# Kernel tuning notes

Measured on AMD Instinct MI355X. Metric: run time of the kernel, lower is better.

The kernel has to match this reference:

```python
import jax, jax.numpy as jnp
import numpy as np

NUM_ATTRS = 8    # A: number of attribute names in attr_map
NUM_VALS = 16    # V: number of distinct values per attribute


def setup_inputs() -> dict:
    key = jax.random.key(0)
    k1, k2 = jax.random.split(key)
    B, D = 2_000_000, 8
    predictions = jax.random.normal(k1, (B, D), dtype=jnp.float32)
    attr_vals = jax.random.randint(k2, (B, NUM_ATTRS), 0, NUM_VALS, dtype=jnp.int32)
    return {"predictions": predictions, "attr_vals": attr_vals}


def reference(predictions, attr_vals):
    B, A = attr_vals.shape
    V = NUM_VALS
    # per-node mean of sigmoid probs; stacking rows then .mean() == mean of per-node means
    per_node = jnp.mean(jax.nn.sigmoid(predictions), axis=1)  # [B]
    # flatten (attr, value) groups into A*V segments
    seg_ids = (attr_vals + jnp.arange(A, dtype=attr_vals.dtype)[None, :] * V).reshape(-1)  # [B*A]
    vals = jnp.broadcast_to(per_node[:, None], (B, A)).reshape(-1)  # [B*A]
    sums = jax.ops.segment_sum(vals, seg_ids, num_segments=A * V)
    counts = jax.ops.segment_sum(jnp.ones_like(vals), seg_ids, num_segments=A * V)
    means = (sums / jnp.maximum(counts, 1.0)).reshape(A, V)      # [A, V]
    present = (counts > 0).reshape(A, V)                          # [A, V]
    # pairwise squared diffs of group means within each attribute (i < j)
    diff = means[:, :, None] - means[:, None, :]                  # [A, V, V]
    triu = jnp.triu(jnp.ones((V, V), dtype=bool), k=1)
    pair_mask = present[:, :, None] & present[:, None, :] & triu[None, :, :]
    total_loss = jnp.sum(jnp.where(pair_mask, diff * diff, 0.0))
    num_comparisons = jnp.sum(pair_mask)
    return jnp.where(num_comparisons > 0, total_loss / num_comparisons, 0.0)
```

## Files before the change

### kernel.cpp

```cpp
#include <hip/hip_runtime.h>

#define NA 8
#define NV 16
#define NS (NA * NV)
#define NP 4
#define NJ 256
#define NE (NP * NJ)
#define FIX_SHIFT 43
#define FIX_MASK ((1ULL << FIX_SHIFT) - 1)
#define FIX_SCALE 2147483648.0f

__global__ __launch_bounds__(256) void k1_accum(
    const float4* __restrict__ preds4,
    const int4*   __restrict__ attrs4,
    unsigned long long* __restrict__ partials,
    int total4, int nb)
{
    __shared__ unsigned long long h[NE];
    for (int i = threadIdx.x; i < NE; i += 256) h[i] = 0ULL;
    __syncthreads();

    const int pbase = (threadIdx.x & 1) ? 2 * NJ : 0;
    const int stride = nb * 256;
    for (int idx = blockIdx.x * 256 + threadIdx.x; idx < total4; idx += stride) {
        float4 p = preds4[idx];
        int4   a = attrs4[idx];

        float half = __builtin_amdgcn_rcpf(1.0f + __expf(-p.x))
                   + __builtin_amdgcn_rcpf(1.0f + __expf(-p.y))
                   + __builtin_amdgcn_rcpf(1.0f + __expf(-p.z))
                   + __builtin_amdgcn_rcpf(1.0f + __expf(-p.w));
        float per_node = (half + __shfl_xor(half, 1)) * 0.125f;
        unsigned int fixed = (unsigned int)(per_node * FIX_SCALE);
        unsigned long long add = (1ULL << FIX_SHIFT) | (unsigned long long)fixed;

        atomicAdd(&h[pbase + ((a.x << 4) | a.y)], add);
        atomicAdd(&h[pbase + NJ + ((a.z << 4) | a.w)], add);
    }
    __syncthreads();

    unsigned long long* dst = partials + (size_t)blockIdx.x * NE;
    for (int i = threadIdx.x; i < NE; i += 256) {
        dst[i] = h[i];
    }
}

__global__ __launch_bounds__(256) void k2_reduce(
    const unsigned long long* __restrict__ partials,
    unsigned long long* __restrict__ jsum,
    unsigned int*       __restrict__ jcnt,
    int g)
{
    const unsigned long long* src = partials + (size_t)blockIdx.x * g * NE;
    unsigned long long s0 = 0, s1 = 0, s2 = 0, s3 = 0;
    unsigned int c0 = 0, c1 = 0, c2 = 0, c3 = 0;
    for (int b = 0; b < g; ++b) {
        const unsigned long long* s = src + (size_t)b * NE;
        unsigned long long p0 = s[threadIdx.x];
        unsigned long long p1 = s[threadIdx.x + 256];
        unsigned long long p2 = s[threadIdx.x + 512];
        unsigned long long p3 = s[threadIdx.x + 768];
        s0 += p0 & FIX_MASK; c0 += (unsigned int)(p0 >> FIX_SHIFT);
        s1 += p1 & FIX_MASK; c1 += (unsigned int)(p1 >> FIX_SHIFT);
        s2 += p2 & FIX_MASK; c2 += (unsigned int)(p2 >> FIX_SHIFT);
        s3 += p3 & FIX_MASK; c3 += (unsigned int)(p3 >> FIX_SHIFT);
    }
    atomicAdd(&jsum[threadIdx.x],       s0);
    atomicAdd(&jsum[threadIdx.x + 256], s1);
    atomicAdd(&jsum[threadIdx.x + 512], s2);
    atomicAdd(&jsum[threadIdx.x + 768], s3);
    atomicAdd(&jcnt[threadIdx.x],       c0);
    atomicAdd(&jcnt[threadIdx.x + 256], c1);
    atomicAdd(&jcnt[threadIdx.x + 512], c2);
    atomicAdd(&jcnt[threadIdx.x + 768], c3);
}

__global__ __launch_bounds__(128) void k3_finalize(
    const unsigned long long* __restrict__ jsum,
    const unsigned int*       __restrict__ jcnt,
    float* __restrict__ out)
{
    __shared__ double s_mean[NS];
    __shared__ int    s_pres[NS];

    const int t = threadIdx.x;
    const int a = t >> 4;
    const int v = t & (NV - 1);
    const int p = a >> 1;

    unsigned long long S = 0ULL;
    unsigned int C = 0u;
    if ((a & 1) == 0) {
        for (int j = 0; j < NV; ++j) {
            const int e = p * NJ + (v << 4) + j;
            S += jsum[e]; C += jcnt[e];
        }
    } else {
        for (int i = 0; i < NV; ++i) {
            const int e = p * NJ + (i << 4) + v;
            S += jsum[e]; C += jcnt[e];
        }
    }
    s_pres[t] = (C > 0u) ? 1 : 0;
    s_mean[t] = (C > 0u)
        ? ((double)S * (1.0 / (double)FIX_SCALE)) / (double)C : 0.0;
    __syncthreads();

    double loss = 0.0;
    int    ncmp = 0;
    if (s_pres[t]) {
        const double mi = s_mean[t];
        for (int j = v + 1; j < NV; ++j) {
            const int sj = (a << 4) + j;
            if (s_pres[sj]) {
                const double d = mi - s_mean[sj];
                loss += d * d;
                ncmp += 1;
            }
        }
    }
    for (int off = 32; off > 0; off >>= 1) {
        loss += __shfl_down(loss, off, 64);
        ncmp += __shfl_down(ncmp, off, 64);
    }
    __shared__ double w_loss[2];
    __shared__ int    w_ncmp[2];
    const int wave = t >> 6;
    if ((t & 63) == 0) { w_loss[wave] = loss; w_ncmp[wave] = ncmp; }
    __syncthreads();
    if (t == 0) {
        const double total = w_loss[0] + w_loss[1];
        const int    n     = w_ncmp[0] + w_ncmp[1];
        out[0] = (n > 0) ? (float)(total / (double)n) : 0.0f;
    }
}

extern "C" void kernel_launch(void* const* d_in, const int* in_sizes, int n_in,
                              void* d_out, int out_size, void* d_ws, size_t ws_size,
                              hipStream_t stream) {
    const float4* preds4 = (const float4*)d_in[0];
    const int4*   attrs4 = (const int4*)d_in[1];
    float*        out    = (float*)d_out;

    const int B = in_sizes[1] / NA;
    const int total4 = B * 2;

    const size_t tail = (size_t)NE * (sizeof(unsigned long long) + sizeof(unsigned int));
    int nb = 2048;
    while (nb > 256 &&
           (size_t)nb * NE * sizeof(unsigned long long) + tail > ws_size) {
        nb >>= 1;
    }

    unsigned long long* partials = (unsigned long long*)d_ws;
    unsigned long long* jsum = partials + (size_t)nb * NE;
    unsigned int*       jcnt = (unsigned int*)(jsum + NE);

    hipMemsetAsync(jsum, 0, tail, stream);
    k1_accum<<<nb, 256, 0, stream>>>(preds4, attrs4, partials, total4, nb);
    k2_reduce<<<nb / 8, 256, 0, stream>>>(partials, jsum, jcnt, 8);
    k3_finalize<<<1, 128, 0, stream>>>(jsum, jcnt, out);
}
```

Baseline: 161.2 us.

## Batch four loads per thread, use DPP for pair sum, halve grid

The accumulation loop now loads four float4/int4 pairs up front before doing any compute or shared-memory atomics, so more memory requests are in flight per thread. The cross-lane pair sum uses a DPP quad-permute move instead of __shfl_xor, which avoids the LDS-based shuffle path. The block count drops from 2048 to 1024, which halves the per-block partials written and reduced by the later kernels but leaves fewer waves to hide latency. Keeping four loads live raises register pressure.

```diff
diff --git a/kernel.cpp b/kernel.cpp
--- a/kernel.cpp
+++ b/kernel.cpp
@@ -10,6 +10,25 @@
 #define FIX_MASK ((1ULL << FIX_SHIFT) - 1)
 #define FIX_SCALE 2147483648.0f
 
+__device__ __forceinline__ float xor1_add(float x) {
+    int y = __builtin_amdgcn_mov_dpp(__float_as_int(x), 0xB1, 0xF, 0xF, true);
+    return x + __int_as_float(y);
+}
+
+__device__ __forceinline__ void process_half(
+    float4 p, int4 a, int pbase, unsigned long long* h)
+{
+    float halfsum = __builtin_amdgcn_rcpf(1.0f + __expf(-p.x))
+                  + __builtin_amdgcn_rcpf(1.0f + __expf(-p.y))
+                  + __builtin_amdgcn_rcpf(1.0f + __expf(-p.z))
+                  + __builtin_amdgcn_rcpf(1.0f + __expf(-p.w));
+    float per_node = xor1_add(halfsum) * 0.125f;
+    unsigned int fixed = (unsigned int)(per_node * FIX_SCALE);
+    unsigned long long add = (1ULL << FIX_SHIFT) | (unsigned long long)fixed;
+    atomicAdd(&h[pbase + ((a.x << 4) | a.y)], add);
+    atomicAdd(&h[pbase + NJ + ((a.z << 4) | a.w)], add);
+}
+
 __global__ __launch_bounds__(256) void k1_accum(
     const float4* __restrict__ preds4,
     const int4*   __restrict__ attrs4,
@@ -21,21 +40,27 @@
     __syncthreads();
 
     const int pbase = (threadIdx.x & 1) ? 2 * NJ : 0;
-    const int stride = nb * 256;
-    for (int idx = blockIdx.x * 256 + threadIdx.x; idx < total4; idx += stride) {
-        float4 p = preds4[idx];
-        int4   a = attrs4[idx];
+    const int stride  = nb * 256;
+    const int stride4 = stride * 4;
 
-        float half = __builtin_amdgcn_rcpf(1.0f + __expf(-p.x))
-                   + __builtin_amdgcn_rcpf(1.0f + __expf(-p.y))
-                   + __builtin_amdgcn_rcpf(1.0f + __expf(-p.z))
-                   + __builtin_amdgcn_rcpf(1.0f + __expf(-p.w));
-        float per_node = (half + __shfl_xor(half, 1)) * 0.125f;
-        unsigned int fixed = (unsigned int)(per_node * FIX_SCALE);
-        unsigned long long add = (1ULL << FIX_SHIFT) | (unsigned long long)fixed;
+    for (int base = blockIdx.x * 256 + threadIdx.x; base < total4; base += stride4) {
+        const int i1 = base + stride;
+        const int i2 = base + 2 * stride;
+        const int i3 = base + 3 * stride;
+        const bool b1 = i1 < total4, b2 = i2 < total4, b3 = i3 < total4;
 
-        atomicAdd(&h[pbase + ((a.x << 4) | a.y)], add);
-        atomicAdd(&h[pbase + NJ + ((a.z << 4) | a.w)], add);
+        float4 p0 = preds4[base];
+        int4   a0 = attrs4[base];
+        float4 p1, p2, p3;
+        int4   a1, a2, a3;
+        if (b1) { p1 = preds4[i1]; a1 = attrs4[i1]; }
+        if (b2) { p2 = preds4[i2]; a2 = attrs4[i2]; }
+        if (b3) { p3 = preds4[i3]; a3 = attrs4[i3]; }
+
+        process_half(p0, a0, pbase, h);
+        if (b1) process_half(p1, a1, pbase, h);
+        if (b2) process_half(p2, a2, pbase, h);
+        if (b3) process_half(p3, a3, pbase, h);
     }
     __syncthreads();
 
@@ -146,7 +171,7 @@
     const int total4 = B * 2;
 
     const size_t tail = (size_t)NE * (sizeof(unsigned long long) + sizeof(unsigned int));
-    int nb = 2048;
+    int nb = 1024;
     while (nb > 256 &&
            (size_t)nb * NE * sizeof(unsigned long long) + tail > ws_size) {
         nb >>= 1;
```

New measurement: 152.2 us. 1.06x faster.
